# Performance work log

Measured on AMD Instinct MI355X. Metric: run time of the kernel, lower is better.

## Reference

```python
import jax, jax.numpy as jnp
import numpy as np

D_MODEL = 768
NUM_HEADS = 12
D_K = D_MODEL // NUM_HEADS


def setup_inputs() -> dict:
    key = jax.random.key(0)
    ks = jax.random.split(key, 9)
    B, N, C = 32, 577, D_MODEL
    s = 1.0 / np.sqrt(C)
    x = jax.random.normal(ks[0], (B, N, C), dtype=jnp.float32)
    Wq = jax.random.normal(ks[1], (C, C), dtype=jnp.float32) * s
    bq = jnp.zeros((C,), dtype=jnp.float32)
    Wk = jax.random.normal(ks[2], (C, C), dtype=jnp.float32) * s
    bk = jnp.zeros((C,), dtype=jnp.float32)
    Wv = jax.random.normal(ks[3], (C, C), dtype=jnp.float32) * s
    bv = jnp.zeros((C,), dtype=jnp.float32)
    Wo = jax.random.normal(ks[4], (C, C), dtype=jnp.float32) * s
    bo = jnp.zeros((C,), dtype=jnp.float32)
    return {"x": x, "Wq": Wq, "bq": bq, "Wk": Wk, "bk": bk,
            "Wv": Wv, "bv": bv, "Wo": Wo, "bo": bo}


def reference(x, Wq, bq, Wk, bk, Wv, bv, Wo, bo):
    B, N, C = x.shape
    H, dk = NUM_HEADS, D_K
    # Linear projections (torch Linear: x @ W.T + b)
    q = (x @ Wq.T + bq).reshape(B, N, H, dk).transpose(0, 2, 1, 3)  # [B,H,N,dk]
    k = (x @ Wk.T + bk).reshape(B, N, H, dk).transpose(0, 2, 1, 3)
    v = (x @ Wv.T + bv).reshape(B, N, H, dk).transpose(0, 2, 1, 3)
    scale = 1.0 / jnp.sqrt(jnp.asarray(dk, dtype=x.dtype))
    scores = jnp.einsum('bhnd,bhmd->bhnm', q, k) * scale  # [B,H,N,N]
    attn = jax.nn.softmax(scores, axis=-1)
    out = jnp.einsum('bhnm,bhmd->bhnd', attn, v)  # [B,H,N,dk]
    out = out.transpose(0, 2, 1, 3).reshape(B, N, C)
    return out @ Wo.T + bo
```

## Files before the change

### kernel.cpp

```cpp
#include <hip/hip_runtime.h>
#include <cstdint>
#include <cstddef>

typedef float  f32x4   __attribute__((ext_vector_type(4)));
typedef __bf16 bf16x8  __attribute__((ext_vector_type(8)));
typedef short  short8  __attribute__((ext_vector_type(8)));
typedef short  short4v __attribute__((ext_vector_type(4)));
typedef float  float4v __attribute__((ext_vector_type(4)));

#define DEVI __device__ __forceinline__

constexpr int Bb = 32, Nn = 577, Cc = 768, Hh = 12, DK = 64;
constexpr int Mm   = Bb * Nn;
constexpr int NQKV = 3 * Cc;
constexpr int NKPAD = 640;
constexpr int NT = 10;
#define QSCALE 0.1803368926f

DEVI short f2bf(float f) {
  __bf16 h = (__bf16)f;
  short s;
  __builtin_memcpy(&s, &h, 2);
  return s;
}

DEVI void gload16(const short* g, short* l) {
  __builtin_amdgcn_global_load_lds(
      (const __attribute__((address_space(1))) void*)g,
      (__attribute__((address_space(3))) void*)l, 16, 0, 0);
}

DEVI f32x4 mfma16(bf16x8 a, bf16x8 b, f32x4 c) {
  return __builtin_amdgcn_mfma_f32_16x16x32_bf16(a, b, c, 0, 0, 0);
}

DEVI void remap_grouped(int bid, int nbm, int nbn, int GM, int& bm, int& bn) {
  const int nwg = nbm * nbn;
  const int xcd = bid & 7, j = bid >> 3;
  const int q = nwg >> 3, r = nwg & 7;
  int wg = (xcd < r ? xcd * (q + 1) : r * (q + 1) + (xcd - r) * q) + j;
  const int per = GM * nbn;
  int grp = wg / per;
  int first = grp * GM;
  int sz = min(GM, nbm - first);
  int rem = wg - grp * per;
  bm = first + rem % sz;
  bn = rem / sz;
}


__global__ void k_cvt(const float* __restrict__ in, short* __restrict__ out, int n4) {
  int i = blockIdx.x * 256 + threadIdx.x;
  if (i >= n4) return;
  float4v v = *(const float4v*)(in + (size_t)i * 4);
  short4v o;
#pragma unroll
  for (int j = 0; j < 4; ++j) o[j] = f2bf(v[j]);
  *(short4v*)(out + (size_t)i * 4) = o;
}

__global__ void k_cvt_wqkv(const float* __restrict__ Wq, const float* __restrict__ Wk,
                           const float* __restrict__ Wv, short* __restrict__ out) {
  int i = blockIdx.x * 256 + threadIdx.x;
  int e = i * 4;
  if (e >= NQKV * Cc) return;
  const int WSZ = Cc * Cc;
  const float* src;
  if (e < WSZ)          src = Wq + e;
  else if (e < 2 * WSZ) src = Wk + (e - WSZ);
  else                  src = Wv + (e - 2 * WSZ);
  float4v v = *(const float4v*)src;
  short4v o;
#pragma unroll
  for (int j = 0; j < 4; ++j) o[j] = f2bf(v[j]);
  *(short4v*)(out + (size_t)e) = o;
}

#define WAITV(N) asm volatile("s_waitcnt vmcnt(" #N ")" ::: "memory")

#define PHASE(DKH, MH, STAGE_STMT, WAIT_STMT)                              \
  {                                                                        \
    const short* Ab_ = Al + (DKH) * 8192;                                  \
    const short* Bb_ = Bl + (DKH) * 8192;                                  \
    bf16x8 af_[4];                                                         \
    _Pragma("unroll")                                                      \
    for (int m_ = 0; m_ < 4; ++m_)                                         \
      af_[m_] = *(const bf16x8*)(Ab_ + offA[(MH) * 4 + m_]);               \
    if ((MH) == 0) {                                                       \
      _Pragma("unroll")                                                    \
      for (int n_ = 0; n_ < 4; ++n_)                                       \
        bfr[n_] = *(const bf16x8*)(Bb_ + offB[n_]);                        \
    }                                                                      \
    STAGE_STMT;                                                            \
    WAIT_STMT;                                                             \
    __builtin_amdgcn_s_barrier();                                          \
    __builtin_amdgcn_s_setprio(1);                                         \
    _Pragma("unroll")                                                      \
    for (int m_ = 0; m_ < 4; ++m_)                                         \
      _Pragma("unroll")                                                    \
      for (int n_ = 0; n_ < 4; ++n_)                                       \
        acc[(MH) * 4 + m_][n_] = mfma16(af_[m_], bfr[n_], acc[(MH) * 4 + m_][n_]); \
    __builtin_amdgcn_s_setprio(0);                                         \
    __builtin_amdgcn_s_barrier();                                          \
  }

DEVI void gemm256_core(const short* __restrict__ A, const short* __restrict__ Bm,
                       int arows, int bm, int bn,
                       short* Al, short* Bl, f32x4 acc[8][4]) {
  const int tid = threadIdx.x;
  const int lane = tid & 63, w = tid >> 6;
  const int wm = w >> 2, wn = w & 3;
  const int qi = lane & 15, g = lane >> 4;

#pragma unroll
  for (int m = 0; m < 8; ++m)
#pragma unroll
    for (int n = 0; n < 4; ++n) acc[m][n] = (f32x4)0.0f;

  const int r0 = tid >> 2, gq = tid & 3;
  const int gs0 = (gq ^ ((r0 + (r0 >> 2)) & 3)) * 8;
  int ga0 = bm * 256 + r0;       if (ga0 > arows - 1) ga0 = arows - 1;
  int ga1 = bm * 256 + 128 + r0; if (ga1 > arows - 1) ga1 = arows - 1;
  const short* pA0 = A  + (size_t)ga0 * Cc + gs0;
  const short* pA1 = A  + (size_t)ga1 * Cc + gs0;
  const short* pB0 = Bm + (size_t)(bn * 256 + r0) * Cc + gs0;
  const short* pB1 = Bm + (size_t)(bn * 256 + 128 + r0) * Cc + gs0;

  auto stA = [&](int dkh, int coff) {
    short* d = Al + dkh * 8192 + w * 512;
    gload16(pA0 + coff, d);
    gload16(pA1 + coff, d + 4096);
  };
  auto stB = [&](int dkh, int coff) {
    short* d = Bl + dkh * 8192 + w * 512;
    gload16(pB0 + coff, d);
    gload16(pB1 + coff, d + 4096);
  };

  int offA[8], offB[4];
#pragma unroll
  for (int m = 0; m < 8; ++m) {
    int r = wm * 128 + m * 16 + qi;
    offA[m] = r * 32 + ((g ^ ((r + (r >> 2)) & 3)) * 8);
  }
#pragma unroll
  for (int n = 0; n < 4; ++n) {
    int r = wn * 64 + n * 16 + qi;
    offB[n] = r * 32 + ((g ^ ((r + (r >> 2)) & 3)) * 8);
  }
  bf16x8 bfr[4];

  stA(0, 0);  stB(0, 0);
  stA(1, 32); stB(1, 32);
  stA(2, 64); stB(2, 64);
  WAITV(4);
  __builtin_amdgcn_s_barrier();

#pragma unroll 1
  for (int i = 0; i < 5; ++i) {
    const int ko = i * 128;
    PHASE(0, 0, stA(3, ko + 96),  (void)0);
    PHASE(0, 1, stB(3, ko + 96),  WAITV(8));
    PHASE(1, 0, stA(0, ko + 128), (void)0);
    PHASE(1, 1, stB(0, ko + 128), WAITV(8));
    PHASE(2, 0, stA(1, ko + 160), (void)0);
    PHASE(2, 1, stB(1, ko + 160), WAITV(8));
    PHASE(3, 0, stA(2, ko + 192), (void)0);
    PHASE(3, 1, stB(2, ko + 192), WAITV(8));
  }
  PHASE(0, 0, stA(3, 736), (void)0);
  PHASE(0, 1, stB(3, 736), WAITV(8));
  PHASE(1, 0, (void)0, (void)0);
  PHASE(1, 1, (void)0, WAITV(4));
  PHASE(2, 0, (void)0, (void)0);
  PHASE(2, 1, (void)0, WAITV(0));
  PHASE(3, 0, (void)0, (void)0);
  PHASE(3, 1, (void)0, (void)0);
}

__global__ __launch_bounds__(512) void k_gemm_qkv(
    const short* __restrict__ A, const short* __restrict__ Bm,
    const float* __restrict__ bq, const float* __restrict__ bk, const float* __restrict__ bv,
    short* __restrict__ qv, short* __restrict__ kv, short* __restrict__ vv) {
  __shared__ short Al[4 * 8192];
  __shared__ short Bl[4 * 8192];
  int bm, bn;
  remap_grouped((int)blockIdx.x, (Mm + 255) / 256, NQKV / 256, 4, bm, bn);
  f32x4 acc[8][4];
  gemm256_core(A, Bm, Mm, bm, bn, Al, Bl, acc);

  const int lane = threadIdx.x & 63, w = threadIdx.x >> 6;
  const int wm = w >> 2, wn = w & 3;
  const int qi = lane & 15, g = lane >> 4;
  const int cb = bn * 256 + wn * 64;
  const int proj = cb / Cc;
  const int within = cb - proj * Cc;
  const float* bias = proj == 0 ? bq : proj == 1 ? bk : bv;
  short* dst = proj == 0 ? qv : proj == 1 ? kv : vv;
  const float sc = proj == 0 ? QSCALE : 1.0f;
  const int hh = within >> 6;
  float bvv[4];
#pragma unroll
  for (int n = 0; n < 4; ++n) bvv[n] = bias[within + n * 16 + qi];
#pragma unroll
  for (int m = 0; m < 8; ++m)
#pragma unroll
    for (int r = 0; r < 4; ++r) {
      int row = bm * 256 + wm * 128 + m * 16 + g * 4 + r;
      if (row < Mm) {
        int b = row / Nn;
        int nn = row - b * Nn;
        size_t base = ((size_t)(b * Hh + hh) * Nn + nn) * DK;
#pragma unroll
        for (int n = 0; n < 4; ++n)
          dst[base + n * 16 + qi] = f2bf((acc[m][n][r] + bvv[n]) * sc);
      }
    }
}

__global__ __launch_bounds__(512) void k_gemm_out(
    const short* __restrict__ A, const short* __restrict__ Bm,
    const float* __restrict__ bo, float* __restrict__ out) {
  __shared__ short Al[4 * 8192];
  __shared__ short Bl[4 * 8192];
  int bm, bn;
  remap_grouped((int)blockIdx.x, (Mm + 255) / 256, Cc / 256, 8, bm, bn);
  f32x4 acc[8][4];
  gemm256_core(A, Bm, Mm, bm, bn, Al, Bl, acc);

  const int lane = threadIdx.x & 63, w = threadIdx.x >> 6;
  const int wm = w >> 2, wn = w & 3;
  const int qi = lane & 15, g = lane >> 4;
  const int cb = bn * 256 + wn * 64;
  float bvv[4];
#pragma unroll
  for (int n = 0; n < 4; ++n) bvv[n] = bo[cb + n * 16 + qi];
#pragma unroll
  for (int m = 0; m < 8; ++m)
#pragma unroll
    for (int r = 0; r < 4; ++r) {
      int row = bm * 256 + wm * 128 + m * 16 + g * 4 + r;
      if (row < Mm) {
#pragma unroll
        for (int n = 0; n < 4; ++n)
          out[(size_t)row * Cc + cb + n * 16 + qi] = acc[m][n][r] + bvv[n];
      }
    }
}

__global__ __launch_bounds__(256) void k_transpose_v(const short* __restrict__ v,
                                                     short* __restrict__ vt) {
  __shared__ short t[64 * 72];
  const int bid = blockIdx.x;
  const int ch = bid % NT, bh = bid / NT;
  const int tid = threadIdx.x;
  const short* vb = v + (size_t)bh * Nn * DK;
#pragma unroll
  for (int i = 0; i < 2; ++i) {
    int gi = i * 256 + tid;
    int r = gi >> 3, c = gi & 7;
    int n = ch * 64 + r;
    short8 val;
#pragma unroll
    for (int j = 0; j < 8; ++j) val[j] = 0;
    if (n < Nn) val = *(const short8*)(vb + (size_t)n * DK + c * 8);
    *(short8*)(t + r * 72 + c * 8) = val;
  }
  __syncthreads();
  short* ob = vt + (size_t)bh * DK * NKPAD + ch * 64;
#pragma unroll
  for (int i = 0; i < 2; ++i) {
    int gi = i * 256 + tid;
    int d = gi >> 3, cg = gi & 7;
    short8 o;
#pragma unroll
    for (int j = 0; j < 8; ++j) o[j] = t[(cg * 8 + j) * 72 + d];
    *(short8*)(ob + (size_t)d * NKPAD + cg * 8) = o;
  }
}

__global__ __launch_bounds__(256) void k_attn(const short* __restrict__ q,
                                              const short* __restrict__ k,
                                              const short* __restrict__ vt,
                                              short* __restrict__ ao) {
  __shared__ short Ks[2][64 * 64];
  __shared__ short Vs[2][64 * 64];
  __shared__ short Ps[4][2][16 * 64];
  int bid = (int)blockIdx.x;
  bid = (bid & 7) * 240 + (bid >> 3);
  const int qtp = bid % 5, bh = bid / 5;
  const int qt0 = qtp * 2;
  const int bb = bh / Hh, hh = bh - bb * Hh;
  const int tid = threadIdx.x, lane = tid & 63, w = tid >> 6;
  const int qi = lane & 15, g = lane >> 4;

  const short* qb  = q  + (size_t)bh * Nn * DK;
  const short* kb  = k  + (size_t)bh * Nn * DK;
  const short* vtb = vt + (size_t)bh * DK * NKPAD;

  const int qrow = qt0 * 64 + w * 16 + qi;
  const bf16x8 qf0a = *(const bf16x8*)(qb + (size_t)qrow * DK + g * 8);
  const bf16x8 qf1a = *(const bf16x8*)(qb + (size_t)qrow * DK + 32 + g * 8);
  const bf16x8 qf0b = *(const bf16x8*)(qb + (size_t)(qrow + 64) * DK + g * 8);
  const bf16x8 qf1b = *(const bf16x8*)(qb + (size_t)(qrow + 64) * DK + 32 + g * 8);

  const int r0 = tid >> 3, cc = tid & 7;
  const int cs0 = (cc ^ (r0 & 7)) * 8;
  const short* kg = kb + r0 * DK + cs0;
  const short* vg = vtb + (size_t)r0 * NKPAD + cs0;
  short* const Kd0 = &Ks[0][w * 512]; short* const Kd1 = &Ks[1][w * 512];
  short* const Vd0 = &Vs[0][w * 512]; short* const Vd1 = &Vs[1][w * 512];

  auto stage = [&](short* Kd, short* Vd) {
    gload16(kg, Kd);          gload16(kg + 2048,  Kd + 2048);
    gload16(vg, Vd);          gload16(vg + 20480, Vd + 2048);
    kg += 4096;               vg += 64;
  };

  const int swq = qi & 7;
  const short* const KF00 = &Ks[0][qi * 64 + ((g    ) ^ swq) * 8];
  const short* const KF01 = &Ks[0][qi * 64 + ((g + 4) ^ swq) * 8];
  const short* const KF10 = &Ks[1][qi * 64 + ((g    ) ^ swq) * 8];
  const short* const KF11 = &Ks[1][qi * 64 + ((g + 4) ^ swq) * 8];
  const short* const VF00 = &Vs[0][qi * 64 + ((g    ) ^ swq) * 8];
  const short* const VF01 = &Vs[0][qi * 64 + ((g + 4) ^ swq) * 8];
  const short* const VF10 = &Vs[1][qi * 64 + ((g    ) ^ swq) * 8];
  const short* const VF11 = &Vs[1][qi * 64 + ((g + 4) ^ swq) * 8];
  const int pwo0 = qi * 64 + (((0  + g) ^ (swq << 1)) << 2);
  const int pwo1 = qi * 64 + (((4  + g) ^ (swq << 1)) << 2);
  const int pwo2 = qi * 64 + (((8  + g) ^ (swq << 1)) << 2);
  const int pwo3 = qi * 64 + (((12 + g) ^ (swq << 1)) << 2);
  const int pro0 = qi * 64 + ((g    ) ^ swq) * 8;
  const int pro1 = qi * 64 + ((g + 4) ^ swq) * 8;
  short* const PA = &Ps[w][0][0];
  short* const PB = &Ps[w][1][0];

  f32x4 accA[4], accB[4];
#pragma unroll
  for (int nd = 0; nd < 4; ++nd) { accA[nd] = (f32x4)0.0f; accB[nd] = (f32x4)0.0f; }
  float lsA = 0.f, lsB = 0.f;

  auto smax = [&](f32x4* s, float& ls, short* P, bool last) {
    if (last) {
#pragma unroll
      for (int ni = 0; ni < 4; ++ni)
#pragma unroll
        for (int r = 0; r < 4; ++r)
          if (ni || r) s[ni][r] = -1e30f;
      if (g) s[0][0] = -1e30f;
    }
    float rs = 0.f;
    short4v pk0, pk1, pk2, pk3;
#pragma unroll
    for (int r = 0; r < 4; ++r) { float p = exp2f(s[0][r]); rs += p; pk0[r] = f2bf(p); }
#pragma unroll
    for (int r = 0; r < 4; ++r) { float p = exp2f(s[1][r]); rs += p; pk1[r] = f2bf(p); }
#pragma unroll
    for (int r = 0; r < 4; ++r) { float p = exp2f(s[2][r]); rs += p; pk2[r] = f2bf(p); }
#pragma unroll
    for (int r = 0; r < 4; ++r) { float p = exp2f(s[3][r]); rs += p; pk3[r] = f2bf(p); }
    *(short4v*)(P + pwo0) = pk0; *(short4v*)(P + pwo1) = pk1;
    *(short4v*)(P + pwo2) = pk2; *(short4v*)(P + pwo3) = pk3;
    rs += __shfl_xor(rs, 16);
    rs += __shfl_xor(rs, 32);
    ls += rs;
  };

  auto tilestep = [&](const short* Kf0, const short* Kf1,
                      const short* Vf0, const short* Vf1, bool last) {
    f32x4 sA[4], sB[4];
#pragma unroll
    for (int ni = 0; ni < 4; ++ni) { sA[ni] = (f32x4)0.0f; sB[ni] = (f32x4)0.0f; }
    {
      bf16x8 kf[4];
#pragma unroll
      for (int ni = 0; ni < 4; ++ni) kf[ni] = *(const bf16x8*)(Kf0 + ni * 1024);
#pragma unroll
      for (int ni = 0; ni < 4; ++ni) sA[ni] = mfma16(kf[ni], qf0a, sA[ni]);
#pragma unroll
      for (int ni = 0; ni < 4; ++ni) sB[ni] = mfma16(kf[ni], qf0b, sB[ni]);
#pragma unroll
      for (int ni = 0; ni < 4; ++ni) kf[ni] = *(const bf16x8*)(Kf1 + ni * 1024);
#pragma unroll
      for (int ni = 0; ni < 4; ++ni) sA[ni] = mfma16(kf[ni], qf1a, sA[ni]);
#pragma unroll
      for (int ni = 0; ni < 4; ++ni) sB[ni] = mfma16(kf[ni], qf1b, sB[ni]);
    }
    smax(sA, lsA, PA, last);
    smax(sB, lsB, PB, last);
    bf16x8 paA0 = *(const bf16x8*)(PA + pro0);
    bf16x8 paA1 = *(const bf16x8*)(PA + pro1);
    bf16x8 paB0 = *(const bf16x8*)(PB + pro0);
    bf16x8 paB1 = *(const bf16x8*)(PB + pro1);
    {
      bf16x8 vf[4];
#pragma unroll
      for (int nd = 0; nd < 4; ++nd) vf[nd] = *(const bf16x8*)(Vf0 + nd * 1024);
#pragma unroll
      for (int nd = 0; nd < 4; ++nd) accA[nd] = mfma16(paA0, vf[nd], accA[nd]);
#pragma unroll
      for (int nd = 0; nd < 4; ++nd) accB[nd] = mfma16(paB0, vf[nd], accB[nd]);
#pragma unroll
      for (int nd = 0; nd < 4; ++nd) vf[nd] = *(const bf16x8*)(Vf1 + nd * 1024);
#pragma unroll
      for (int nd = 0; nd < 4; ++nd) accA[nd] = mfma16(paA1, vf[nd], accA[nd]);
#pragma unroll
      for (int nd = 0; nd < 4; ++nd) accB[nd] = mfma16(paB1, vf[nd], accB[nd]);
    }
  };

  stage(Kd0, Vd0);
  __syncthreads();
#pragma unroll 1
  for (int t2 = 0; t2 < 5; ++t2) {
    stage(Kd1, Vd1);
    tilestep(KF00, KF01, VF00, VF01, false);
    __syncthreads();
    if (t2 < 4) {
      stage(Kd0, Vd0);
      tilestep(KF10, KF11, VF10, VF11, false);
      __syncthreads();
    }
  }
  tilestep(KF10, KF11, VF10, VF11, true);

  auto epi = [&](f32x4* accd, float ls, int qt) {
    float ls4[4];
#pragma unroll
    for (int r = 0; r < 4; ++r) ls4[r] = __shfl(ls, (g << 2) + r);
#pragma unroll
    for (int r = 0; r < 4; ++r) {
      int qr = qt * 64 + w * 16 + (g << 2) + r;
      if (qr < Nn) {
        float inv = 1.0f / ls4[r];
        size_t base = ((size_t)(bb * Nn + qr)) * Cc + hh * DK;
#pragma unroll
        for (int nd = 0; nd < 4; ++nd)
          ao[base + nd * 16 + qi] = f2bf(accd[nd][r] * inv);
      }
    }
  };
  epi(accA, lsA, qt0);
  epi(accB, lsB, qt0 + 1);
}


extern "C" void kernel_launch(void* const* d_in, const int* in_sizes, int n_in,
                              void* d_out, int out_size, void* d_ws, size_t ws_size,
                              hipStream_t stream) {
  const float* x  = (const float*)d_in[0];
  const float* Wq = (const float*)d_in[1];
  const float* bq = (const float*)d_in[2];
  const float* Wk = (const float*)d_in[3];
  const float* bk = (const float*)d_in[4];
  const float* Wv = (const float*)d_in[5];
  const float* bv = (const float*)d_in[6];
  const float* Wo = (const float*)d_in[7];
  const float* bo = (const float*)d_in[8];
  float* out = (float*)d_out;

  char* ws = (char*)d_ws;
  size_t off = 0;
  auto alloc = [&](size_t bytes) {
    char* p = ws + off;
    off += (bytes + 255) & ~(size_t)255;
    return p;
  };
  short* xb   = (short*)alloc((size_t)Mm * Cc * 2);
  short* wqkv = (short*)alloc((size_t)NQKV * Cc * 2);
  short* wob  = (short*)alloc((size_t)Cc * Cc * 2);
  short* qb   = (short*)alloc((size_t)Bb * Hh * Nn * DK * 2);
  short* kb   = (short*)alloc((size_t)Bb * Hh * Nn * DK * 2);
  short* vb   = (short*)alloc((size_t)Bb * Hh * Nn * DK * 2);
  short* vtb  = (short*)alloc((size_t)Bb * Hh * DK * NKPAD * 2);
  short* aob  = xb;

  k_cvt<<<(Mm * Cc / 4 + 255) / 256, 256, 0, stream>>>(x, xb, Mm * Cc / 4);
  k_cvt_wqkv<<<(NQKV * Cc / 4 + 255) / 256, 256, 0, stream>>>(Wq, Wk, Wv, wqkv);
  k_cvt<<<(Cc * Cc / 4 + 255) / 256, 256, 0, stream>>>(Wo, wob, Cc * Cc / 4);

  const int nbm = (Mm + 255) / 256;
  k_gemm_qkv<<<nbm * (NQKV / 256), 512, 0, stream>>>(xb, wqkv, bq, bk, bv, qb, kb, vb);

  k_transpose_v<<<Bb * Hh * NT, 256, 0, stream>>>(vb, vtb);

  k_attn<<<Bb * Hh * 5, 256, 0, stream>>>(qb, kb, vtb, aob);

  k_gemm_out<<<nbm * (Cc / 256), 512, 0, stream>>>(aob, wob, bo, out);
}
```

Before: 223.9 us.

## Restructure GEMM LDS pipeline to double-buffered 64-wide K tiles; share P buffer

The shared GEMM core for the QKV and output projections moves from four 32-wide K stages to two 64-wide K buffers. It uses a new XOR swizzle (row&7) and interleaves the global-to-LDS loads across eight sub-phases with retuned vmcnt waits. This is meant to cut pipeline bookkeeping and use wider LDS rows for bank-conflict-free reads, at the cost of a shallower prefetch depth. The attention kernel also halves its per-wave P scratch by reusing one buffer for both query halves, reading A's probabilities before writing B's. That saves LDS but serializes the two softmax halves through the same memory.

```diff
diff --git a/kernel.cpp b/kernel.cpp
--- a/kernel.cpp
+++ b/kernel.cpp
@@ -78,21 +78,21 @@
 
 #define WAITV(N) asm volatile("s_waitcnt vmcnt(" #N ")" ::: "memory")
 
-#define PHASE(DKH, MH, STAGE_STMT, WAIT_STMT)                              \
+#define GPH(BUF, KK, MH, STAGE, WAIT)                                      \
   {                                                                        \
-    const short* Ab_ = Al + (DKH) * 8192;                                  \
-    const short* Bb_ = Bl + (DKH) * 8192;                                  \
+    const short* Ab_ = Al + (BUF) * 16384;                                 \
+    const short* Bb_ = Bl + (BUF) * 16384;                                 \
     bf16x8 af_[4];                                                         \
     _Pragma("unroll")                                                      \
     for (int m_ = 0; m_ < 4; ++m_)                                         \
-      af_[m_] = *(const bf16x8*)(Ab_ + offA[(MH) * 4 + m_]);               \
+      af_[m_] = *(const bf16x8*)(Ab_ + (offA[(MH) * 4 + m_] ^ ((KK) * 32))); \
     if ((MH) == 0) {                                                       \
       _Pragma("unroll")                                                    \
       for (int n_ = 0; n_ < 4; ++n_)                                       \
-        bfr[n_] = *(const bf16x8*)(Bb_ + offB[n_]);                        \
+        bfr[n_] = *(const bf16x8*)(Bb_ + (offB[n_] ^ ((KK) * 32)));        \
     }                                                                      \
-    STAGE_STMT;                                                            \
-    WAIT_STMT;                                                             \
+    STAGE;                                                                 \
+    WAIT;                                                                  \
     __builtin_amdgcn_s_barrier();                                          \
     __builtin_amdgcn_s_setprio(1);                                         \
     _Pragma("unroll")                                                      \
@@ -104,9 +104,9 @@
     __builtin_amdgcn_s_barrier();                                          \
   }
 
-DEVI void gemm256_core(const short* __restrict__ A, const short* __restrict__ Bm,
-                       int arows, int bm, int bn,
-                       short* Al, short* Bl, f32x4 acc[8][4]) {
+DEVI void gemm256b(const short* __restrict__ A, const short* __restrict__ Bm,
+                   int arows, int bm, int bn,
+                   short* Al, short* Bl, f32x4 acc[8][4]) {
   const int tid = threadIdx.x;
   const int lane = tid & 63, w = tid >> 6;
   const int wm = w >> 2, wn = w & 3;
@@ -117,77 +117,76 @@
 #pragma unroll
     for (int n = 0; n < 4; ++n) acc[m][n] = (f32x4)0.0f;
 
-  const int r0 = tid >> 2, gq = tid & 3;
-  const int gs0 = (gq ^ ((r0 + (r0 >> 2)) & 3)) * 8;
-  int ga0 = bm * 256 + r0;       if (ga0 > arows - 1) ga0 = arows - 1;
-  int ga1 = bm * 256 + 128 + r0; if (ga1 > arows - 1) ga1 = arows - 1;
-  const short* pA0 = A  + (size_t)ga0 * Cc + gs0;
-  const short* pA1 = A  + (size_t)ga1 * Cc + gs0;
-  const short* pB0 = Bm + (size_t)(bn * 256 + r0) * Cc + gs0;
-  const short* pB1 = Bm + (size_t)(bn * 256 + 128 + r0) * Cc + gs0;
-
-  auto stA = [&](int dkh, int coff) {
-    short* d = Al + dkh * 8192 + w * 512;
-    gload16(pA0 + coff, d);
-    gload16(pA1 + coff, d + 4096);
-  };
-  auto stB = [&](int dkh, int coff) {
-    short* d = Bl + dkh * 8192 + w * 512;
-    gload16(pB0 + coff, d);
-    gload16(pB1 + coff, d + 4096);
+  const int rloc = tid >> 3, c8 = tid & 7;
+  const int gswz = (c8 ^ (rloc & 7)) * 8;
+  const short* pA[4];
+  const short* pB[4];
+#pragma unroll
+  for (int s = 0; s < 4; ++s) {
+    int ra = bm * 256 + s * 64 + rloc; if (ra > arows - 1) ra = arows - 1;
+    pA[s] = A  + (size_t)ra * Cc + gswz;
+    pB[s] = Bm + (size_t)(bn * 256 + s * 64 + rloc) * Cc + gswz;
+  }
+  auto stA = [&](int buf, int s, int co) {
+    gload16(pA[s] + co, Al + buf * 16384 + s * 4096 + tid * 8);
+  };
+  auto stB = [&](int buf, int s, int co) {
+    gload16(pB[s] + co, Bl + buf * 16384 + s * 4096 + tid * 8);
   };
 
   int offA[8], offB[4];
 #pragma unroll
   for (int m = 0; m < 8; ++m) {
     int r = wm * 128 + m * 16 + qi;
-    offA[m] = r * 32 + ((g ^ ((r + (r >> 2)) & 3)) * 8);
+    offA[m] = r * 64 + ((g ^ (r & 7)) * 8);
   }
 #pragma unroll
   for (int n = 0; n < 4; ++n) {
     int r = wn * 64 + n * 16 + qi;
-    offB[n] = r * 32 + ((g ^ ((r + (r >> 2)) & 3)) * 8);
+    offB[n] = r * 64 + ((g ^ (r & 7)) * 8);
   }
   bf16x8 bfr[4];
 
-  stA(0, 0);  stB(0, 0);
-  stA(1, 32); stB(1, 32);
-  stA(2, 64); stB(2, 64);
-  WAITV(4);
+  stA(0, 0, 0); stA(0, 1, 0); stA(0, 2, 0); stA(0, 3, 0);
+  stB(0, 0, 0); stB(0, 1, 0); stB(0, 2, 0); stB(0, 3, 0);
+  stB(1, 0, 64); stB(1, 1, 64);
+  WAITV(2);
   __builtin_amdgcn_s_barrier();
 
 #pragma unroll 1
   for (int i = 0; i < 5; ++i) {
-    const int ko = i * 128;
-    PHASE(0, 0, stA(3, ko + 96),  (void)0);
-    PHASE(0, 1, stB(3, ko + 96),  WAITV(8));
-    PHASE(1, 0, stA(0, ko + 128), (void)0);
-    PHASE(1, 1, stB(0, ko + 128), WAITV(8));
-    PHASE(2, 0, stA(1, ko + 160), (void)0);
-    PHASE(2, 1, stB(1, ko + 160), WAITV(8));
-    PHASE(3, 0, stA(2, ko + 192), (void)0);
-    PHASE(3, 1, stB(2, ko + 192), WAITV(8));
-  }
-  PHASE(0, 0, stA(3, 736), (void)0);
-  PHASE(0, 1, stB(3, 736), WAITV(8));
-  PHASE(1, 0, (void)0, (void)0);
-  PHASE(1, 1, (void)0, WAITV(4));
-  PHASE(2, 0, (void)0, (void)0);
-  PHASE(2, 1, (void)0, WAITV(0));
-  PHASE(3, 0, (void)0, (void)0);
-  PHASE(3, 1, (void)0, (void)0);
+    const int cb1  = 64 + 128 * i;
+    const int cb0n = cb1 + 64;
+    const int cb1n = cb1 + 128;
+    GPH(0, 0, 0, (stB(1, 2, cb1),  stB(1, 3, cb1)),  (void)0);
+    GPH(0, 0, 1, (stA(1, 0, cb1),  stA(1, 2, cb1)),  (void)0);
+    GPH(0, 1, 0, (stA(1, 1, cb1),  stA(1, 3, cb1)),  (void)0);
+    GPH(0, 1, 1, (stA(0, 0, cb0n), stA(0, 2, cb0n)), WAITV(4));
+    GPH(1, 0, 0, (stA(0, 1, cb0n), stA(0, 3, cb0n)), WAITV(4));
+    GPH(1, 0, 1, (stB(0, 0, cb0n), stB(0, 1, cb0n)), (void)0);
+    GPH(1, 1, 0, (stB(0, 2, cb0n), stB(0, 3, cb0n)), (void)0);
+    GPH(1, 1, 1, (stB(1, 0, cb1n), stB(1, 1, cb1n)), WAITV(2));
+  }
+  GPH(0, 0, 0, (stB(1, 2, 704), stB(1, 3, 704)), (void)0);
+  GPH(0, 0, 1, (stA(1, 0, 704), stA(1, 2, 704)), (void)0);
+  GPH(0, 1, 0, (stA(1, 1, 704), stA(1, 3, 704)), (void)0);
+  GPH(0, 1, 1, (void)0, WAITV(2));
+  GPH(1, 0, 0, (void)0, WAITV(0));
+  GPH(1, 0, 1, (void)0, (void)0);
+  GPH(1, 1, 0, (void)0, (void)0);
+  GPH(1, 1, 1, (void)0, (void)0);
 }
 
 __global__ __launch_bounds__(512) void k_gemm_qkv(
     const short* __restrict__ A, const short* __restrict__ Bm,
     const float* __restrict__ bq, const float* __restrict__ bk, const float* __restrict__ bv,
     short* __restrict__ qv, short* __restrict__ kv, short* __restrict__ vv) {
-  __shared__ short Al[4 * 8192];
-  __shared__ short Bl[4 * 8192];
+  __shared__ short Al[2 * 16384];
+  __shared__ short Bl[2 * 16384];
   int bm, bn;
   remap_grouped((int)blockIdx.x, (Mm + 255) / 256, NQKV / 256, 4, bm, bn);
   f32x4 acc[8][4];
-  gemm256_core(A, Bm, Mm, bm, bn, Al, Bl, acc);
+  gemm256b(A, Bm, Mm, bm, bn, Al, Bl, acc);
 
   const int lane = threadIdx.x & 63, w = threadIdx.x >> 6;
   const int wm = w >> 2, wn = w & 3;
@@ -221,12 +220,12 @@
 __global__ __launch_bounds__(512) void k_gemm_out(
     const short* __restrict__ A, const short* __restrict__ Bm,
     const float* __restrict__ bo, float* __restrict__ out) {
-  __shared__ short Al[4 * 8192];
-  __shared__ short Bl[4 * 8192];
+  __shared__ short Al[2 * 16384];
+  __shared__ short Bl[2 * 16384];
   int bm, bn;
   remap_grouped((int)blockIdx.x, (Mm + 255) / 256, Cc / 256, 8, bm, bn);
   f32x4 acc[8][4];
-  gemm256_core(A, Bm, Mm, bm, bn, Al, Bl, acc);
+  gemm256b(A, Bm, Mm, bm, bn, Al, Bl, acc);
 
   const int lane = threadIdx.x & 63, w = threadIdx.x >> 6;
   const int wm = w >> 2, wn = w & 3;
@@ -285,7 +284,7 @@
                                               short* __restrict__ ao) {
   __shared__ short Ks[2][64 * 64];
   __shared__ short Vs[2][64 * 64];
-  __shared__ short Ps[4][2][16 * 64];
+  __shared__ short Ps[4][16 * 64];
   int bid = (int)blockIdx.x;
   bid = (bid & 7) * 240 + (bid >> 3);
   const int qtp = bid % 5, bh = bid / 5;
@@ -326,21 +325,19 @@
   const short* const VF01 = &Vs[0][qi * 64 + ((g + 4) ^ swq) * 8];
   const short* const VF10 = &Vs[1][qi * 64 + ((g    ) ^ swq) * 8];
   const short* const VF11 = &Vs[1][qi * 64 + ((g + 4) ^ swq) * 8];
-  const int pwo0 = qi * 64 + (((0  + g) ^ (swq << 1)) << 2);
-  const int pwo1 = qi * 64 + (((4  + g) ^ (swq << 1)) << 2);
-  const int pwo2 = qi * 64 + (((8  + g) ^ (swq << 1)) << 2);
-  const int pwo3 = qi * 64 + (((12 + g) ^ (swq << 1)) << 2);
-  const int pro0 = qi * 64 + ((g    ) ^ swq) * 8;
-  const int pro1 = qi * 64 + ((g + 4) ^ swq) * 8;
-  short* const PA = &Ps[w][0][0];
-  short* const PB = &Ps[w][1][0];
+  short* const PW0 = &Ps[w][qi * 64 + (((0  + g) ^ (swq << 1)) << 2)];
+  short* const PW1 = &Ps[w][qi * 64 + (((4  + g) ^ (swq << 1)) << 2)];
+  short* const PW2 = &Ps[w][qi * 64 + (((8  + g) ^ (swq << 1)) << 2)];
+  short* const PW3 = &Ps[w][qi * 64 + (((12 + g) ^ (swq << 1)) << 2)];
+  const short* const PR0 = &Ps[w][qi * 64 + ((g    ) ^ swq) * 8];
+  const short* const PR1 = &Ps[w][qi * 64 + ((g + 4) ^ swq) * 8];
 
   f32x4 accA[4], accB[4];
 #pragma unroll
   for (int nd = 0; nd < 4; ++nd) { accA[nd] = (f32x4)0.0f; accB[nd] = (f32x4)0.0f; }
   float lsA = 0.f, lsB = 0.f;
 
-  auto smax = [&](f32x4* s, float& ls, short* P, bool last) {
+  auto smax = [&](f32x4* s, float& ls, bool last) {
     if (last) {
 #pragma unroll
       for (int ni = 0; ni < 4; ++ni)
@@ -359,8 +356,8 @@
     for (int r = 0; r < 4; ++r) { float p = exp2f(s[2][r]); rs += p; pk2[r] = f2bf(p); }
 #pragma unroll
     for (int r = 0; r < 4; ++r) { float p = exp2f(s[3][r]); rs += p; pk3[r] = f2bf(p); }
-    *(short4v*)(P + pwo0) = pk0; *(short4v*)(P + pwo1) = pk1;
-    *(short4v*)(P + pwo2) = pk2; *(short4v*)(P + pwo3) = pk3;
+    *(short4v*)PW0 = pk0; *(short4v*)PW1 = pk1;
+    *(short4v*)PW2 = pk2; *(short4v*)PW3 = pk3;
     rs += __shfl_xor(rs, 16);
     rs += __shfl_xor(rs, 32);
     ls += rs;
@@ -386,12 +383,12 @@
 #pragma unroll
       for (int ni = 0; ni < 4; ++ni) sB[ni] = mfma16(kf[ni], qf1b, sB[ni]);
     }
-    smax(sA, lsA, PA, last);
-    smax(sB, lsB, PB, last);
-    bf16x8 paA0 = *(const bf16x8*)(PA + pro0);
-    bf16x8 paA1 = *(const bf16x8*)(PA + pro1);
-    bf16x8 paB0 = *(const bf16x8*)(PB + pro0);
-    bf16x8 paB1 = *(const bf16x8*)(PB + pro1);
+    smax(sA, lsA, last);
+    bf16x8 paA0 = *(const bf16x8*)PR0;
+    bf16x8 paA1 = *(const bf16x8*)PR1;
+    smax(sB, lsB, last);
+    bf16x8 paB0 = *(const bf16x8*)PR0;
+    bf16x8 paB1 = *(const bf16x8*)PR1;
     {
       bf16x8 vf[4];
 #pragma unroll
```

New measurement: 215.8 us. 3.6% less time.
